# Performance work log

Measured on AMD Instinct MI355X. Metric: run time of the kernel, lower is better.

Reference implementation:

```python
import jax, jax.numpy as jnp
import numpy as np

N_NODES = 40000
N_EDGES = 640000
D = 128  # in_channels == out_channels (required by the module's math)


def setup_inputs() -> dict:
    key = jax.random.key(0)
    ks = jax.random.split(key, 8)
    s = 1.0 / np.sqrt(D)  # torch Linear default init scale
    x = jax.random.normal(ks[0], (N_NODES, D), dtype=jnp.float32)
    edge_index = jax.random.randint(ks[1], (2, N_EDGES), 0, N_NODES, dtype=jnp.int64)
    Wn_w = jax.random.uniform(ks[2], (D, D), jnp.float32, -s, s)
    Wn_b = jax.random.uniform(ks[3], (D,), jnp.float32, -s, s)
    Wg_w = jax.random.uniform(ks[4], (D, D), jnp.float32, -s, s)
    Wg_b = jax.random.uniform(ks[5], (D,), jnp.float32, -s, s)
    Wa_w = jax.random.uniform(ks[6], (D, D), jnp.float32, -s, s)
    Wa_b = jax.random.uniform(ks[7], (D,), jnp.float32, -s, s)
    return {"x": x, "edge_index": edge_index,
            "Wn_w": Wn_w, "Wn_b": Wn_b,
            "Wg_w": Wg_w, "Wg_b": Wg_b,
            "Wa_w": Wa_w, "Wa_b": Wa_b}


def reference(x, edge_index, Wn_w, Wn_b, Wg_w, Wg_b, Wa_w, Wa_b):
    row, col = edge_index[0], edge_index[1]
    x_col = x[col]                                  # [E, D] gather
    alpha = jax.nn.sigmoid(x_col @ Wa_w + Wa_b)     # [E, D] edge attention
    neigh = x_col * alpha                           # [E, D]
    aggr = jax.ops.segment_sum(neigh, row, num_segments=x.shape[0])  # [N, D]
    out = jnp.tanh((x @ Wn_w + Wn_b) + (aggr @ Wg_w + Wg_b))
    return out  # dropout p=0.0 is identity
```

## Files before the change

### kernel.cpp

```cpp
#include <hip/hip_runtime.h>

#define NN 40000
#define NE 640000
#define D 128
#define CAP 64

typedef __attribute__((ext_vector_type(8))) short short8;
typedef __attribute__((ext_vector_type(4))) float f32x4;
typedef __attribute__((ext_vector_type(4))) int i32x4;

__device__ __forceinline__ short f2b(float v) {
  unsigned int u = __builtin_bit_cast(unsigned int, v);
  u = (u + 0x7fffu + ((u >> 16) & 1u)) >> 16;
  return (short)u;
}
__device__ __forceinline__ float b2f(short s) {
  unsigned int u = ((unsigned int)(unsigned short)s) << 16;
  return __builtin_bit_cast(float, u);
}

__global__ __launch_bounds__(256) void k_prep(
    const float* __restrict__ Wn, const float* __restrict__ Wg,
    const float* __restrict__ Wa, short* __restrict__ WnT,
    short* __restrict__ WgThi, short* __restrict__ WgTlo,
    short* __restrict__ WaT, int* __restrict__ cnt, short* __restrict__ h) {
  int i = blockIdx.x * 256 + threadIdx.x;
  int k = i >> 7, c = i & 127;
  WnT[c * D + k] = f2b(Wn[k * D + c]);
  WaT[c * D + k] = f2b(Wa[k * D + c]);
  float v = Wg[k * D + c];
  short hi = f2b(v);
  WgThi[c * D + k] = hi;
  WgTlo[c * D + k] = f2b(v - b2f(hi));
  if (i < 10000) {
    i32x4 z = {0, 0, 0, 0};
    *(i32x4*)(cnt + i * 4) = z;
  }
  if (i < 16) {
    short8 z = {0, 0, 0, 0, 0, 0, 0, 0};
    *(short8*)(h + (size_t)NN * D + i * 8) = z;
  }
}

__global__ __launch_bounds__(256) void k_fill(
    const int* __restrict__ ei, int* __restrict__ cnt,
    int* __restrict__ bucket) {
  int e = blockIdx.x * 256 + threadIdx.x;
  if (e >= NE) return;
  int r = ei[e];
  int c = ei[NE + e];
  int slot = atomicAdd(&cnt[r], 1);
  if (slot < CAP) bucket[r * CAP + slot] = c;
}

__global__ __launch_bounds__(256) void k_node(
    const float* __restrict__ x, const short* __restrict__ WaT,
    const float* __restrict__ ba, short* __restrict__ h_out,
    short* __restrict__ xbf_out) {
  __shared__ float al_s[16][132];
  int r0 = blockIdx.x * 16;
  int w = threadIdx.x >> 6, l = threadIdx.x & 63;
  int g = l >> 4, c16 = l & 15;
  int rowA = r0 + c16;

  f32x4 xf[8];
  short8 a[4];
#pragma unroll
  for (int kt = 0; kt < 4; ++kt) {
    const float* p = x + (size_t)rowA * D + kt * 32 + g * 8;
    f32x4 v0 = *(const f32x4*)p;
    f32x4 v1 = *(const f32x4*)(p + 4);
    xf[kt * 2] = v0;
    xf[kt * 2 + 1] = v1;
    short8 t;
    t[0] = f2b(v0[0]); t[1] = f2b(v0[1]); t[2] = f2b(v0[2]); t[3] = f2b(v0[3]);
    t[4] = f2b(v1[0]); t[5] = f2b(v1[1]); t[6] = f2b(v1[2]); t[7] = f2b(v1[3]);
    a[kt] = t;
    *(short8*)(xbf_out + (size_t)rowA * D + kt * 32 + g * 8) = t;
  }

#pragma unroll
  for (int u = 0; u < 2; ++u) {
    int ct = w * 2 + u;
    int cc = ct * 16 + c16;
    f32x4 c = {0.f, 0.f, 0.f, 0.f};
#pragma unroll
    for (int kt = 0; kt < 4; ++kt) {
      short8 b = *(const short8*)(WaT + (size_t)cc * D + kt * 32 + g * 8);
      c = __builtin_amdgcn_mfma_f32_16x16x32_bf16(a[kt], b, c, 0, 0, 0);
    }
    float bav = ba[cc];
#pragma unroll
    for (int r = 0; r < 4; ++r) {
      float t = c[r] + bav;
      al_s[g * 4 + r][cc] = 1.0f / (1.0f + __expf(-t));
    }
  }
  __syncthreads();

  short8 hh;
#pragma unroll
  for (int q = 0; q < 8; ++q) {
    float av = al_s[c16][w * 32 + g * 8 + q];
    float xv = xf[w * 2 + (q >> 2)][q & 3];
    hh[q] = f2b(xv * av);
  }
  *(short8*)(h_out + (size_t)rowA * D + w * 32 + g * 8) = hh;
}

__global__ __launch_bounds__(512) void k_fused(
    const int* __restrict__ cnt, const int* __restrict__ bucket,
    const short* __restrict__ h, const short* __restrict__ xbf,
    const short* __restrict__ WnT, const short* __restrict__ WgThi,
    const short* __restrict__ WgTlo, const float* __restrict__ bn,
    const float* __restrict__ bg, float* __restrict__ out) {
  __shared__ float st[16][132];
  int w = threadIdx.x >> 6, l = threadIdx.x & 63;
  int g = l >> 4, i = l & 15;
  int base = blockIdx.x * 16;

  {
    int n0 = base + 2 * w, n1 = n0 + 1;
    int deg0 = cnt[n0]; deg0 = deg0 < CAP ? deg0 : CAP;
    int deg1 = cnt[n1]; deg1 = deg1 < CAP ? deg1 : CAP;
    int dmax = deg0 > deg1 ? deg0 : deg1;
    float a0[8], a1[8];
#pragma unroll
    for (int q = 0; q < 8; ++q) { a0[q] = 0.f; a1[q] = 0.f; }

    for (int j = 0; j < dmax; j += 16) {
      i32x4 idx0 = *(const i32x4*)(bucket + (size_t)n0 * CAP + j + 4 * g);
      i32x4 idx1 = *(const i32x4*)(bucket + (size_t)n1 * CAP + j + 4 * g);
      short8 v0[4], v1[4];
#pragma unroll
      for (int k = 0; k < 4; ++k) {
        int slot = j + 4 * g + k;
        int r0c = slot < deg0 ? idx0[k] : NN;
        int r1c = slot < deg1 ? idx1[k] : NN;
        v0[k] = *(const short8*)(h + (size_t)r0c * D + i * 8);
        v1[k] = *(const short8*)(h + (size_t)r1c * D + i * 8);
      }
#pragma unroll
      for (int k = 0; k < 4; ++k) {
#pragma unroll
        for (int q = 0; q < 8; ++q) {
          a0[q] += b2f(v0[k][q]);
          a1[q] += b2f(v1[k][q]);
        }
      }
    }
#pragma unroll
    for (int q = 0; q < 8; ++q) {
      a0[q] += __shfl_xor(a0[q], 16);
      a0[q] += __shfl_xor(a0[q], 32);
      a1[q] += __shfl_xor(a1[q], 16);
      a1[q] += __shfl_xor(a1[q], 32);
    }
    if (g == 0) {
      f32x4 lo = {a0[0], a0[1], a0[2], a0[3]};
      f32x4 hi = {a0[4], a0[5], a0[6], a0[7]};
      *(f32x4*)&st[w * 2][i * 8] = lo;
      *(f32x4*)&st[w * 2][i * 8 + 4] = hi;
    } else if (g == 1) {
      f32x4 lo = {a1[0], a1[1], a1[2], a1[3]};
      f32x4 hi = {a1[4], a1[5], a1[6], a1[7]};
      *(f32x4*)&st[w * 2 + 1][i * 8] = lo;
      *(f32x4*)&st[w * 2 + 1][i * 8 + 4] = hi;
    }
  }
  __syncthreads();

  int rowG = base + i;
  int cc = w * 16 + i;
  f32x4 c = {0.f, 0.f, 0.f, 0.f};
  float bias = bn[cc] + bg[cc];
#pragma unroll
  for (int kt = 0; kt < 4; ++kt) {
    short8 axf = *(const short8*)(xbf + (size_t)rowG * D + kt * 32 + g * 8);
    const float* p = &st[i][kt * 32 + g * 8];
    f32x4 v0 = *(const f32x4*)p;
    f32x4 v1 = *(const f32x4*)(p + 4);
    short8 sh, sl;
#pragma unroll
    for (int jq = 0; jq < 4; ++jq) {
      short hh = f2b(v0[jq]);
      sh[jq] = hh;
      sl[jq] = f2b(v0[jq] - b2f(hh));
    }
#pragma unroll
    for (int jq = 0; jq < 4; ++jq) {
      short hh = f2b(v1[jq]);
      sh[4 + jq] = hh;
      sl[4 + jq] = f2b(v1[jq] - b2f(hh));
    }
    short8 bwn = *(const short8*)(WnT + (size_t)cc * D + kt * 32 + g * 8);
    short8 bh = *(const short8*)(WgThi + (size_t)cc * D + kt * 32 + g * 8);
    short8 bl = *(const short8*)(WgTlo + (size_t)cc * D + kt * 32 + g * 8);
    c = __builtin_amdgcn_mfma_f32_16x16x32_bf16(axf, bwn, c, 0, 0, 0);
    c = __builtin_amdgcn_mfma_f32_16x16x32_bf16(sh, bh, c, 0, 0, 0);
    c = __builtin_amdgcn_mfma_f32_16x16x32_bf16(sl, bh, c, 0, 0, 0);
    c = __builtin_amdgcn_mfma_f32_16x16x32_bf16(sh, bl, c, 0, 0, 0);
  }
#pragma unroll
  for (int r = 0; r < 4; ++r) {
    int rr = base + g * 4 + r;
    out[(size_t)rr * D + cc] = tanhf(c[r] + bias);
  }
}

extern "C" void kernel_launch(void* const* d_in, const int* in_sizes, int n_in,
                              void* d_out, int out_size, void* d_ws,
                              size_t ws_size, hipStream_t stream) {
  const float* x = (const float*)d_in[0];
  const int* ei = (const int*)d_in[1];
  const float* Wn_w = (const float*)d_in[2];
  const float* Wn_b = (const float*)d_in[3];
  const float* Wg_w = (const float*)d_in[4];
  const float* Wg_b = (const float*)d_in[5];
  const float* Wa_w = (const float*)d_in[6];
  const float* Wa_b = (const float*)d_in[7];

  char* ws = (char*)d_ws;
  short* WaT = (short*)(ws + 0);
  short* WnT = (short*)(ws + 32 * 1024);
  short* WgThi = (short*)(ws + 64 * 1024);
  short* WgTlo = (short*)(ws + 96 * 1024);
  int* cnt = (int*)(ws + 128 * 1024);
  size_t off = 512 * 1024;
  short* h = (short*)(ws + off);
  off += (size_t)(NN + 1) * D * 2;
  short* xbf = (short*)(ws + off);
  off += (size_t)NN * D * 2;
  int* bucket = (int*)(ws + off);
  float* out = (float*)d_out;

  k_prep<<<64, 256, 0, stream>>>(Wn_w, Wg_w, Wa_w, WnT, WgThi, WgTlo, WaT,
                                 cnt, h);
  k_fill<<<(NE + 255) / 256, 256, 0, stream>>>(ei, cnt, bucket);
  k_node<<<NN / 16, 256, 0, stream>>>(x, WaT, Wa_b, h, xbf);
  k_fused<<<2500, 512, 0, stream>>>(cnt, bucket, h, xbf, WnT, WgThi, WgTlo,
                                    Wn_b, Wg_b, out);
}
```

Measured before the change: 128.7 us.

## Fuse edge bucketing into node kernel, use 16-bit buckets and shuffle-broadcast indices

Merges the edge-bucketing pass into the node-attention launch: the first 2500 blocks run the attention work and the next 2500 insert edges into per-node buckets. This removes one kernel launch and lets the two independent phases overlap. Bucket entries are stored as 16-bit indices, which is valid because the node count fits in 16 bits. The gather loop in the fused kernel now loads each node's bucket row once per wave and hands out neighbour indices with wave shuffles, in unrolled steps of two gathers per node. The aim is to cut index-load traffic and latency, at the cost of more shuffles and branches on degree.

```diff
diff --git a/kernel.cpp b/kernel.cpp
--- a/kernel.cpp
+++ b/kernel.cpp
@@ -42,23 +42,22 @@
   }
 }
 
-__global__ __launch_bounds__(256) void k_fill(
-    const int* __restrict__ ei, int* __restrict__ cnt,
-    int* __restrict__ bucket) {
-  int e = blockIdx.x * 256 + threadIdx.x;
-  if (e >= NE) return;
-  int r = ei[e];
-  int c = ei[NE + e];
-  int slot = atomicAdd(&cnt[r], 1);
-  if (slot < CAP) bucket[r * CAP + slot] = c;
-}
-
-__global__ __launch_bounds__(256) void k_node(
+__global__ __launch_bounds__(256) void k_nf(
     const float* __restrict__ x, const short* __restrict__ WaT,
     const float* __restrict__ ba, short* __restrict__ h_out,
-    short* __restrict__ xbf_out) {
+    short* __restrict__ xbf_out, const int* __restrict__ ei,
+    int* __restrict__ cnt, unsigned short* __restrict__ bucket) {
+  int bid = blockIdx.x;
+  if (bid >= 2500) {
+    int e = (bid - 2500) * 256 + threadIdx.x;
+    int r = ei[e];
+    int c = ei[NE + e];
+    int slot = atomicAdd(&cnt[r], 1);
+    if (slot < CAP) bucket[(size_t)r * CAP + slot] = (unsigned short)c;
+    return;
+  }
   __shared__ float al_s[16][132];
-  int r0 = blockIdx.x * 16;
+  int r0 = bid * 16;
   int w = threadIdx.x >> 6, l = threadIdx.x & 63;
   int g = l >> 4, c16 = l & 15;
   int rowA = r0 + c16;
@@ -108,8 +107,25 @@
   *(short8*)(h_out + (size_t)rowA * D + w * 32 + g * 8) = hh;
 }
 
+#define PSTEP(T0, C0A, C0B, C1A, C1B)                               \
+  {                                                                 \
+    int s0 = 4 * (T0) + g, s1 = s0 + 4;                             \
+    int ra0 = s0 < deg0 ? (C0A) : NN;                               \
+    int ra1 = s1 < deg0 ? (C0B) : NN;                               \
+    int rb0 = s0 < deg1 ? (C1A) : NN;                               \
+    int rb1 = s1 < deg1 ? (C1B) : NN;                               \
+    short8 va0 = *(const short8*)(h + (size_t)ra0 * D + i * 8);     \
+    short8 va1 = *(const short8*)(h + (size_t)ra1 * D + i * 8);     \
+    short8 vb0 = *(const short8*)(h + (size_t)rb0 * D + i * 8);     \
+    short8 vb1 = *(const short8*)(h + (size_t)rb1 * D + i * 8);     \
+    _Pragma("unroll") for (int q = 0; q < 8; ++q) {                 \
+      a0[q] += b2f(va0[q]) + b2f(va1[q]);                           \
+      a1[q] += b2f(vb0[q]) + b2f(vb1[q]);                           \
+    }                                                               \
+  }
+
 __global__ __launch_bounds__(512) void k_fused(
-    const int* __restrict__ cnt, const int* __restrict__ bucket,
+    const int* __restrict__ cnt, const unsigned short* __restrict__ bucket,
     const short* __restrict__ h, const short* __restrict__ xbf,
     const short* __restrict__ WnT, const short* __restrict__ WgThi,
     const short* __restrict__ WgTlo, const float* __restrict__ bn,
@@ -124,28 +140,45 @@
     int deg0 = cnt[n0]; deg0 = deg0 < CAP ? deg0 : CAP;
     int deg1 = cnt[n1]; deg1 = deg1 < CAP ? deg1 : CAP;
     int dmax = deg0 > deg1 ? deg0 : deg1;
+    int bc0 = bucket[(size_t)n0 * CAP + l];
+    int bc1 = bucket[(size_t)n1 * CAP + l];
     float a0[8], a1[8];
 #pragma unroll
     for (int q = 0; q < 8; ++q) { a0[q] = 0.f; a1[q] = 0.f; }
 
-    for (int j = 0; j < dmax; j += 16) {
-      i32x4 idx0 = *(const i32x4*)(bucket + (size_t)n0 * CAP + j + 4 * g);
-      i32x4 idx1 = *(const i32x4*)(bucket + (size_t)n1 * CAP + j + 4 * g);
-      short8 v0[4], v1[4];
-#pragma unroll
-      for (int k = 0; k < 4; ++k) {
-        int slot = j + 4 * g + k;
-        int r0c = slot < deg0 ? idx0[k] : NN;
-        int r1c = slot < deg1 ? idx1[k] : NN;
-        v0[k] = *(const short8*)(h + (size_t)r0c * D + i * 8);
-        v1[k] = *(const short8*)(h + (size_t)r1c * D + i * 8);
-      }
-#pragma unroll
-      for (int k = 0; k < 4; ++k) {
+    int c00 = __shfl(bc0, g), c01 = __shfl(bc0, 4 + g);
+    int c02 = __shfl(bc0, 8 + g), c03 = __shfl(bc0, 12 + g);
+    int c10 = __shfl(bc1, g), c11 = __shfl(bc1, 4 + g);
+    int c12 = __shfl(bc1, 8 + g), c13 = __shfl(bc1, 12 + g);
+    PSTEP(0, c00, c01, c10, c11);
+    if (dmax > 8) PSTEP(2, c02, c03, c12, c13);
+    if (dmax > 16) {
+      int c04 = __shfl(bc0, 16 + g), c05 = __shfl(bc0, 20 + g);
+      int c14 = __shfl(bc1, 16 + g), c15 = __shfl(bc1, 20 + g);
+      PSTEP(4, c04, c05, c14, c15);
+    }
+    if (dmax > 24) {
+      int c06 = __shfl(bc0, 24 + g), c07 = __shfl(bc0, 28 + g);
+      int c16_ = __shfl(bc1, 24 + g), c17 = __shfl(bc1, 28 + g);
+      PSTEP(6, c06, c07, c16_, c17);
+    }
+    if (dmax > 32) {
+      for (int j = 32; j < dmax; j += 8) {
+        int s0 = j + g, s1 = j + 4 + g;
+        int d00 = __shfl(bc0, s0 & 63), d01 = __shfl(bc0, s1 & 63);
+        int d10 = __shfl(bc1, s0 & 63), d11 = __shfl(bc1, s1 & 63);
+        int ra0 = s0 < deg0 ? d00 : NN;
+        int ra1 = s1 < deg0 ? d01 : NN;
+        int rb0 = s0 < deg1 ? d10 : NN;
+        int rb1 = s1 < deg1 ? d11 : NN;
+        short8 va0 = *(const short8*)(h + (size_t)ra0 * D + i * 8);
+        short8 va1 = *(const short8*)(h + (size_t)ra1 * D + i * 8);
+        short8 vb0 = *(const short8*)(h + (size_t)rb0 * D + i * 8);
+        short8 vb1 = *(const short8*)(h + (size_t)rb1 * D + i * 8);
 #pragma unroll
         for (int q = 0; q < 8; ++q) {
-          a0[q] += b2f(v0[k][q]);
-          a1[q] += b2f(v1[k][q]);
+          a0[q] += b2f(va0[q]) + b2f(va1[q]);
+          a1[q] += b2f(vb0[q]) + b2f(vb1[q]);
         }
       }
     }
@@ -231,13 +264,12 @@
   off += (size_t)(NN + 1) * D * 2;
   short* xbf = (short*)(ws + off);
   off += (size_t)NN * D * 2;
-  int* bucket = (int*)(ws + off);
+  unsigned short* bucket = (unsigned short*)(ws + off);
   float* out = (float*)d_out;
 
   k_prep<<<64, 256, 0, stream>>>(Wn_w, Wg_w, Wa_w, WnT, WgThi, WgTlo, WaT,
                                  cnt, h);
-  k_fill<<<(NE + 255) / 256, 256, 0, stream>>>(ei, cnt, bucket);
-  k_node<<<NN / 16, 256, 0, stream>>>(x, WaT, Wa_b, h, xbf);
+  k_nf<<<5000, 256, 0, stream>>>(x, WaT, Wa_b, h, xbf, ei, cnt, bucket);
   k_fused<<<2500, 512, 0, stream>>>(cnt, bucket, h, xbf, WnT, WgThi, WgTlo,
                                     Wn_b, Wg_b, out);
 }
```

Measured after the change: 137.2 us. +6.6%, slower.
